# Optimization experiments

Measured on AMD Instinct MI355X. Metric: run time of the kernel, lower is better.

Reference implementation:

```python
import jax, jax.numpy as jnp
import numpy as np

NUM_HEADS = 6

def setup_inputs() -> dict:
    key = jax.random.key(0)
    k1, k2, k3, k4 = jax.random.split(key, 4)
    B, N, C = 8, 2048, 384
    x = jax.random.normal(k1, (B, N, C), dtype=jnp.float32)
    qkv_w = jax.random.normal(k2, (3 * C, C), dtype=jnp.float32) * (C ** -0.5)
    proj_w = jax.random.normal(k3, (C, C), dtype=jnp.float32) * (C ** -0.5)
    proj_b = jax.random.normal(k4, (C,), dtype=jnp.float32) * 0.01
    temperature = jnp.ones((NUM_HEADS, 1, 1), dtype=jnp.float32)
    return {"x": x, "qkv_w": qkv_w, "proj_w": proj_w, "proj_b": proj_b,
            "temperature": temperature}


def reference(x, qkv_w, proj_w, proj_b, temperature):
    B, N, C = x.shape
    H = NUM_HEADS
    Dh = C // H
    # qkv projection (no bias), split into q, k, v per head
    qkv = (x @ qkv_w.T).reshape(B, N, 3, H, Dh)
    qkv = jnp.transpose(qkv, (2, 0, 3, 1, 4))  # [3, B, H, N, Dh]
    q, k, v = qkv[0], qkv[1], qkv[2]
    # scores scaled by sqrt(C) (full dim, as in source), then learnable temperature
    attn = jnp.einsum('bhnd,bhmd->bhnm', q, k) / (C ** 0.5)
    attn = attn / temperature  # temperature: [H,1,1] broadcasts over B and N,N
    # diagonal (self-token) mask -> -inf before softmax
    diag = jnp.eye(N, dtype=bool)
    attn = jnp.where(diag, -jnp.inf, attn)
    attn = jax.nn.softmax(attn, axis=-1)
    # attend and merge heads
    out = jnp.einsum('bhnm,bhmd->bhnd', attn, v)
    out = jnp.transpose(out, (0, 2, 1, 3)).reshape(B, N, C)
    # output projection
    return out @ proj_w.T + proj_b
```

## Files before the change

### kernel.cpp

```cpp
#include <hip/hip_runtime.h>


using f32x4 = __attribute__((ext_vector_type(4))) float;
using s16x8 = __attribute__((ext_vector_type(8))) short;
using u16x4 = __attribute__((ext_vector_type(4))) unsigned short;
using u32x2 = __attribute__((ext_vector_type(2))) unsigned int;
using u32x4 = __attribute__((ext_vector_type(4))) unsigned int;
typedef unsigned short u16;
typedef unsigned int u32;

#define MFMA16(a, b, c) __builtin_amdgcn_mfma_f32_16x16x32_bf16(a, b, c, 0, 0, 0)
#define LOG2E 1.4426950408889634f
#define SQRTC 19.595917942265423f

__device__ __forceinline__ u16 f2bf(float f) {
  u32 u = __float_as_uint(f);
  u += 0x7fffu + ((u >> 16) & 1u);
  return (u16)(u >> 16);
}

__device__ __forceinline__ u32 cvtpk(float lo, float hi) {
  u32 r;
  asm("v_cvt_pk_bf16_f32 %0, %1, %2" : "=v"(r) : "v"(lo), "v"(hi));
  return r;
}

__device__ __forceinline__ float fexp2(float x) {
  float r;
  asm("v_exp_f32 %0, %1" : "=v"(r) : "v"(x));
  return r;
}

__device__ __forceinline__ void gld16(const void* g, void* l) {
  __builtin_amdgcn_global_load_lds((const __attribute__((address_space(1))) void*)g,
                                   (__attribute__((address_space(3))) void*)l, 16, 0, 0);
}

__global__ __launch_bounds__(256) void k_cvt(const float* __restrict__ in,
                                             u16* __restrict__ out) {
  const size_t i = (size_t)blockIdx.x * 256 + threadIdx.x;
  f32x4 v = *(const f32x4*)(in + i * 4);
  u16x4 o;
  o[0] = f2bf(v[0]); o[1] = f2bf(v[1]); o[2] = f2bf(v[2]); o[3] = f2bf(v[3]);
  *(u16x4*)(out + i * 4) = o;
}

__global__ __launch_bounds__(256) void k_qkv(const float* __restrict__ X,
                                             const u16* __restrict__ W,
                                             const float* __restrict__ temp,
                                             u16* __restrict__ Qb,
                                             u16* __restrict__ Kb,
                                             u16* __restrict__ Vt) {
  __shared__ u16 As[2][128 * 32];
  __shared__ u16 Bs[2][128 * 32];
  const int tid = threadIdx.x, w = tid >> 6, l = tid & 63, lr = l & 15, lg = l >> 4;
  const int tn = blockIdx.x * 128, tm = blockIdx.y * 128;
  const int wr = w >> 1, wc = w & 1;
  const int r0 = tid >> 2, c8 = (tid & 3) * 8;
  const int ar = tid >> 1, ac = (tid & 1) * 16;

  f32x4 acc[4][4] = {};
  f32x4 a4[4];

  auto issueA = [&](int kt) {
    const float* xp = X + (size_t)(tm + ar) * 384 + kt * 32 + ac;
    a4[0] = *(const f32x4*)(xp);
    a4[1] = *(const f32x4*)(xp + 4);
    a4[2] = *(const f32x4*)(xp + 8);
    a4[3] = *(const f32x4*)(xp + 12);
  };
  auto commitA = [&](int buf) {
    u32x4 h0, h1;
    h0[0] = cvtpk(a4[0][0], a4[0][1]); h0[1] = cvtpk(a4[0][2], a4[0][3]);
    h0[2] = cvtpk(a4[1][0], a4[1][1]); h0[3] = cvtpk(a4[1][2], a4[1][3]);
    h1[0] = cvtpk(a4[2][0], a4[2][1]); h1[1] = cvtpk(a4[2][2], a4[2][3]);
    h1[2] = cvtpk(a4[3][0], a4[3][1]); h1[3] = cvtpk(a4[3][2], a4[3][3]);
    *(u32x4*)&As[buf][ar * 32 + ac] = h0;
    *(u32x4*)&As[buf][ar * 32 + ac + 8] = h1;
  };
  auto stageB = [&](int buf, int kt) {
    const int k0 = kt * 32;
    char* db = (char*)(&Bs[buf][0]) + (w << 10);
    gld16(W + (size_t)(tn + r0) * 384 + k0 + c8, db);
    gld16(W + (size_t)(tn + 64 + r0) * 384 + k0 + c8, db + 4096);
  };

  issueA(0); stageB(0, 0); commitA(0);
  for (int kt = 0; kt < 12; ++kt) {
    __syncthreads();
    if (kt < 11) { issueA(kt + 1); stageB((kt + 1) & 1, kt + 1); }
    const int buf = kt & 1;
    s16x8 af[4], bfr[4];
    for (int mi = 0; mi < 4; mi++)
      af[mi] = *(const s16x8*)&As[buf][(wr * 64 + mi * 16 + lr) * 32 + lg * 8];
    for (int ni = 0; ni < 4; ni++)
      bfr[ni] = *(const s16x8*)&Bs[buf][(wc * 64 + ni * 16 + lr) * 32 + lg * 8];
    for (int mi = 0; mi < 4; mi++)
      for (int ni = 0; ni < 4; ni++)
        acc[mi][ni] = MFMA16(af[mi], bfr[ni], acc[mi][ni]);
    if (kt < 11) commitA((kt + 1) & 1);
  }

  const int which = (tn + wc * 64) / 384;
  const int bidx = (tm >> 11);
  for (int mi = 0; mi < 4; mi++)
    for (int ni = 0; ni < 4; ni++) {
      const int n = tn + wc * 64 + ni * 16 + lr;
      const int c = n - which * 384;
      const int h = c >> 6, d = c & 63;
      const size_t bh = (size_t)(bidx * 6 + h);
      if (which == 2) {
        const int pos0 = (tm + wr * 64 + mi * 16 + lg * 4) & 2047;
        u16x4 vv;
        vv[0] = f2bf(acc[mi][ni][0]); vv[1] = f2bf(acc[mi][ni][1]);
        vv[2] = f2bf(acc[mi][ni][2]); vv[3] = f2bf(acc[mi][ni][3]);
        *(u16x4*)&Vt[(bh * 64 + d) * 2048 + pos0] = vv;
      } else {
        const float mult = (which == 0) ? (LOG2E / (SQRTC * temp[h])) : 1.0f;
        for (int j = 0; j < 4; j++) {
          const int pos = (tm + wr * 64 + mi * 16 + lg * 4 + j) & 2047;
          const u16 val = f2bf(acc[mi][ni][j] * mult);
          if (which == 0) Qb[(bh * 2048 + pos) * 64 + d] = val;
          else            Kb[(bh * 2048 + pos) * 64 + d] = val;
        }
      }
    }
}

#define LDSOFF(row, c16) (((row) * 128 + (c16) * 16) ^ (((row) & 7) << 4))

__global__ __launch_bounds__(256, 3) void k_attn(const u16* __restrict__ Qb,
                                                 const u16* __restrict__ Kb,
                                                 const u16* __restrict__ Vt,
                                                 u16* __restrict__ AO) {
  __shared__ u16 Ks[2][64 * 64];
  __shared__ u16 Vs[2][64 * 64];
  __shared__ u16 Ps[4][32 * 72];
  const int tid = threadIdx.x, w = tid >> 6, l = tid & 63, lr = l & 15, lg = l >> 4;
  const int orig = blockIdx.x;
  const int rm = (orig & 7) * 96 + (orig >> 3);
  const int qt = rm & 15, bh = rm >> 4;
  const int h = bh % 6, b = bh / 6;
  const size_t base = (size_t)bh << 17;
  const int q0 = qt * 128 + w * 32;
  const int maskKt = q0 >> 6;
  const int qo = q0 & 63;

  s16x8 qf[2][2];
  for (int mi = 0; mi < 2; mi++)
    for (int ks = 0; ks < 2; ks++)
      qf[mi][ks] = *(const s16x8*)&Qb[base + (size_t)(q0 + mi * 16 + lr) * 64 + ks * 32 + lg * 8];

  s16x8 ones;
  for (int e = 0; e < 8; ++e) ones[e] = (short)0x3F80;

  f32x4 o0[4] = {}, o1[4] = {};
  f32x4 os0 = {}, os1 = {};

  const int r0 = tid >> 3, c0 = tid & 7;
  const int c8 = c0 * 8;
  const int wo0 = LDSOFF(r0, c0), wo1 = LDSOFF(r0 + 32, c0);

  s16x8 ka0, ka1, va0, va1;
  auto issue = [&](int kt) {
    const u16* kp = Kb + base + (size_t)(kt * 64 + r0) * 64 + c8;
    ka0 = *(const s16x8*)kp;
    ka1 = *(const s16x8*)(kp + 32 * 64);
    const u16* vp = Vt + base + (size_t)r0 * 2048 + kt * 64 + c8;
    va0 = *(const s16x8*)vp;
    va1 = *(const s16x8*)(vp + 32 * 2048);
  };
  auto commit = [&](int buf) {
    char* kd = (char*)&Ks[buf][0];
    char* vd = (char*)&Vs[buf][0];
    *(s16x8*)(kd + wo0) = ka0; *(s16x8*)(kd + wo1) = ka1;
    *(s16x8*)(vd + wo0) = va0; *(s16x8*)(vd + wo1) = va1;
  };

  issue(0); commit(0);
  __syncthreads();

  const int lrs = (lr & 7) << 4;
  const int x0 = (lg * 16) ^ lrs;
  const int x1 = (64 + lg * 16) ^ lrs;

  for (int kt = 0; kt < 32; ++kt) {
    const int cur = kt & 1;
    if (kt < 31) issue(kt + 1);

    f32x4 st0[4] = {}, st1[4] = {};
    const char* kbp = (const char*)&Ks[cur][0];
    __builtin_amdgcn_s_setprio(1);
    for (int ni = 0; ni < 4; ++ni) {
      const int rb = (ni * 16 + lr) * 128;
      const s16x8 kf0 = *(const s16x8*)(kbp + (rb + x0));
      const s16x8 kf1 = *(const s16x8*)(kbp + (rb + x1));
      st0[ni] = MFMA16(kf0, qf[0][0], st0[ni]);
      st0[ni] = MFMA16(kf1, qf[0][1], st0[ni]);
      st1[ni] = MFMA16(kf0, qf[1][0], st1[ni]);
      st1[ni] = MFMA16(kf1, qf[1][1], st1[ni]);
    }
    __builtin_amdgcn_s_setprio(0);

    if (kt == maskKt) {
      for (int ni = 0; ni < 4; ++ni)
        for (int j = 0; j < 4; ++j) {
          const int kvl = ni * 16 + lg * 4 + j;
          if (kvl == qo + lr)      st0[ni][j] = -1e30f;
          if (kvl == qo + 16 + lr) st1[ni][j] = -1e30f;
        }
    }

    const char* vbp = (const char*)&Vs[cur][0];
    s16x8 vfr[2][4];
    for (int ks = 0; ks < 2; ++ks) {
      const int xk = ks ? x1 : x0;
      for (int dj = 0; dj < 4; ++dj)
        vfr[ks][dj] = *(const s16x8*)(vbp + ((dj * 16 + lr) * 128 + xk));
    }

    u16* const psw = &Ps[w][0];
    {
      u16* pr = psw + lr * 72 + lg * 4;
      for (int ni = 0; ni < 4; ++ni) {
        u32x2 d2;
        d2[0] = cvtpk(fexp2(st0[ni][0]), fexp2(st0[ni][1]));
        d2[1] = cvtpk(fexp2(st0[ni][2]), fexp2(st0[ni][3]));
        *(u32x2*)(pr + ni * 16) = d2;
      }
    }
    {
      const s16x8 pa0k0 = *(const s16x8*)((const char*)(psw + lr * 72) + 0 * 64 + lg * 16);
      const s16x8 pa0k1 = *(const s16x8*)((const char*)(psw + lr * 72) + 1 * 64 + lg * 16);
      __builtin_amdgcn_s_setprio(1);
      for (int dj = 0; dj < 4; ++dj) o0[dj] = MFMA16(pa0k0, vfr[0][dj], o0[dj]);
      os0 = MFMA16(pa0k0, ones, os0);
      for (int dj = 0; dj < 4; ++dj) o0[dj] = MFMA16(pa0k1, vfr[1][dj], o0[dj]);
      os0 = MFMA16(pa0k1, ones, os0);
      __builtin_amdgcn_s_setprio(0);
    }
    {
      u16* pr = psw + (16 + lr) * 72 + lg * 4;
      for (int ni = 0; ni < 4; ++ni) {
        u32x2 d2;
        d2[0] = cvtpk(fexp2(st1[ni][0]), fexp2(st1[ni][1]));
        d2[1] = cvtpk(fexp2(st1[ni][2]), fexp2(st1[ni][3]));
        *(u32x2*)(pr + ni * 16) = d2;
      }
    }
    {
      const s16x8 pa1k0 = *(const s16x8*)((const char*)(psw + (16 + lr) * 72) + 0 * 64 + lg * 16);
      const s16x8 pa1k1 = *(const s16x8*)((const char*)(psw + (16 + lr) * 72) + 1 * 64 + lg * 16);
      __builtin_amdgcn_s_setprio(1);
      for (int dj = 0; dj < 4; ++dj) o1[dj] = MFMA16(pa1k0, vfr[0][dj], o1[dj]);
      os1 = MFMA16(pa1k0, ones, os1);
      for (int dj = 0; dj < 4; ++dj) o1[dj] = MFMA16(pa1k1, vfr[1][dj], o1[dj]);
      os1 = MFMA16(pa1k1, ones, os1);
      __builtin_amdgcn_s_setprio(0);
    }

    if (kt < 31) commit(cur ^ 1);
    __syncthreads();
  }

  f32x4 rv0, rv1;
  for (int j = 0; j < 4; ++j) { rv0[j] = 1.0f / os0[j]; rv1[j] = 1.0f / os1[j]; }
  const size_t aobase = (size_t)b * 2048 * 384 + (size_t)h * 64;
  for (int j = 0; j < 4; ++j) {
    const int pos0 = q0 + lg * 4 + j;
    const int pos1 = pos0 + 16;
    for (int dj = 0; dj < 4; ++dj) {
      AO[aobase + (size_t)pos0 * 384 + dj * 16 + lr] = f2bf(o0[dj][j] * rv0[j]);
      AO[aobase + (size_t)pos1 * 384 + dj * 16 + lr] = f2bf(o1[dj][j] * rv1[j]);
    }
  }
}

__global__ __launch_bounds__(256) void k_proj(const u16* __restrict__ A,
                                              const u16* __restrict__ W,
                                              const float* __restrict__ bias,
                                              float* __restrict__ out) {
  __shared__ u16 As[2][128 * 32];
  __shared__ u16 Bs[2][128 * 32];
  const int tid = threadIdx.x, w = tid >> 6, l = tid & 63, lr = l & 15, lg = l >> 4;
  const int tn = blockIdx.x * 128, tm = blockIdx.y * 128;
  const int wr = w >> 1, wc = w & 1;
  const int r0 = tid >> 2, c8 = (tid & 3) * 8;

  f32x4 acc[4][4] = {};

  auto stage = [&](int buf, int kt) {
    const int k0 = kt * 32;
    char* da = (char*)(&As[buf][0]) + (w << 10);
    char* db = (char*)(&Bs[buf][0]) + (w << 10);
    gld16(A + (size_t)(tm + r0) * 384 + k0 + c8, da);
    gld16(A + (size_t)(tm + 64 + r0) * 384 + k0 + c8, da + 4096);
    gld16(W + (size_t)(tn + r0) * 384 + k0 + c8, db);
    gld16(W + (size_t)(tn + 64 + r0) * 384 + k0 + c8, db + 4096);
  };

  stage(0, 0);
  for (int kt = 0; kt < 12; ++kt) {
    __syncthreads();
    if (kt < 11) stage((kt + 1) & 1, kt + 1);
    const int buf = kt & 1;
    s16x8 af[4], bfr[4];
    for (int mi = 0; mi < 4; mi++)
      af[mi] = *(const s16x8*)&As[buf][(wr * 64 + mi * 16 + lr) * 32 + lg * 8];
    for (int ni = 0; ni < 4; ni++)
      bfr[ni] = *(const s16x8*)&Bs[buf][(wc * 64 + ni * 16 + lr) * 32 + lg * 8];
    for (int mi = 0; mi < 4; mi++)
      for (int ni = 0; ni < 4; ni++)
        acc[mi][ni] = MFMA16(af[mi], bfr[ni], acc[mi][ni]);
  }

  for (int mi = 0; mi < 4; mi++)
    for (int ni = 0; ni < 4; ni++) {
      const int n = tn + wc * 64 + ni * 16 + lr;
      const float bn = bias[n];
      for (int j = 0; j < 4; j++) {
        const int m = tm + wr * 64 + mi * 16 + lg * 4 + j;
        out[(size_t)m * 384 + n] = acc[mi][ni][j] + bn;
      }
    }
}

extern "C" void kernel_launch(void* const* d_in, const int* in_sizes, int n_in,
                              void* d_out, int out_size, void* d_ws, size_t ws_size,
                              hipStream_t stream) {
  const float* x      = (const float*)d_in[0];
  const float* qkv_w  = (const float*)d_in[1];
  const float* proj_w = (const float*)d_in[2];
  const float* proj_b = (const float*)d_in[3];
  const float* temp   = (const float*)d_in[4];
  float* out = (float*)d_out;

  u16* wqkvb  = (u16*)d_ws;
  u16* wprojb = wqkvb + 442368;
  u16* Qb     = wprojb + 147456;
  u16* Kb     = Qb + 6291456;
  u16* Vtb    = Kb + 6291456;
  u16* AOb    = Vtb + 6291456;

  k_cvt<<<432, 256, 0, stream>>>(qkv_w, wqkvb);
  k_cvt<<<144, 256, 0, stream>>>(proj_w, wprojb);
  k_qkv<<<dim3(9, 128), 256, 0, stream>>>(x, wqkvb, temp, Qb, Kb, Vtb);
  k_attn<<<768, 256, 0, stream>>>(Qb, Kb, Vtb, AOb);
  k_proj<<<dim3(3, 128), 256, 0, stream>>>(AOb, wprojb, proj_b, out);
}
```

Measured before the change: 133.3 us.

## Fuse weight casts, transpose Q store, swizzle GEMM grids, shrink proj tile

The two weight-conversion launches are merged into one kernel. The QKV GEMM now writes Q transposed with vectorized 4-element stores, like V, and its block order is swizzled for cache locality. The attention kernel reads Q with strided scalar gathers, but only once per block. The projection GEMM moves to 128x64 tiles with a swizzled grid to double the block count, trading more A reloads for better occupancy and load balance.

Result: faster. 121.8 us (-8.6%).

```diff
diff --git a/kernel.cpp b/kernel.cpp
--- a/kernel.cpp
+++ b/kernel.cpp
@@ -36,9 +36,16 @@
                                    (__attribute__((address_space(3))) void*)l, 16, 0, 0);
 }
 
-__global__ __launch_bounds__(256) void k_cvt(const float* __restrict__ in,
-                                             u16* __restrict__ out) {
-  const size_t i = (size_t)blockIdx.x * 256 + threadIdx.x;
+__global__ __launch_bounds__(256) void k_cvt2(const float* __restrict__ A,
+                                              u16* __restrict__ Oa,
+                                              const float* __restrict__ B,
+                                              u16* __restrict__ Ob) {
+  const int bid = blockIdx.x;
+  const float* in;
+  u16* out;
+  size_t i;
+  if (bid < 432) { in = A; out = Oa; i = (size_t)bid * 256 + threadIdx.x; }
+  else           { in = B; out = Ob; i = (size_t)(bid - 432) * 256 + threadIdx.x; }
   f32x4 v = *(const f32x4*)(in + i * 4);
   u16x4 o;
   o[0] = f2bf(v[0]); o[1] = f2bf(v[1]); o[2] = f2bf(v[2]); o[3] = f2bf(v[3]);
@@ -48,13 +55,15 @@
 __global__ __launch_bounds__(256) void k_qkv(const float* __restrict__ X,
                                              const u16* __restrict__ W,
                                              const float* __restrict__ temp,
-                                             u16* __restrict__ Qb,
+                                             u16* __restrict__ Qt,
                                              u16* __restrict__ Kb,
                                              u16* __restrict__ Vt) {
   __shared__ u16 As[2][128 * 32];
   __shared__ u16 Bs[2][128 * 32];
   const int tid = threadIdx.x, w = tid >> 6, l = tid & 63, lr = l & 15, lg = l >> 4;
-  const int tn = blockIdx.x * 128, tm = blockIdx.y * 128;
+  const int id = blockIdx.y * 9 + blockIdx.x;
+  const int swz = (id & 7) * 144 + (id >> 3);
+  const int tn = (swz % 9) * 128, tm = (swz / 9) * 128;
   const int wr = w >> 1, wc = w & 1;
   const int r0 = tid >> 2, c8 = (tid & 3) * 8;
   const int ar = tid >> 1, ac = (tid & 1) * 16;
@@ -109,27 +118,26 @@
       const int c = n - which * 384;
       const int h = c >> 6, d = c & 63;
       const size_t bh = (size_t)(bidx * 6 + h);
-      if (which == 2) {
+      if (which == 1) {
+        for (int j = 0; j < 4; j++) {
+          const int pos = (tm + wr * 64 + mi * 16 + lg * 4 + j) & 2047;
+          Kb[(bh * 2048 + pos) * 64 + d] = f2bf(acc[mi][ni][j]);
+        }
+      } else {
+        const float mult = (which == 0) ? (LOG2E / (SQRTC * temp[h])) : 1.0f;
         const int pos0 = (tm + wr * 64 + mi * 16 + lg * 4) & 2047;
         u16x4 vv;
-        vv[0] = f2bf(acc[mi][ni][0]); vv[1] = f2bf(acc[mi][ni][1]);
-        vv[2] = f2bf(acc[mi][ni][2]); vv[3] = f2bf(acc[mi][ni][3]);
-        *(u16x4*)&Vt[(bh * 64 + d) * 2048 + pos0] = vv;
-      } else {
-        const float mult = (which == 0) ? (LOG2E / (SQRTC * temp[h])) : 1.0f;
-        for (int j = 0; j < 4; j++) {
-          const int pos = (tm + wr * 64 + mi * 16 + lg * 4 + j) & 2047;
-          const u16 val = f2bf(acc[mi][ni][j] * mult);
-          if (which == 0) Qb[(bh * 2048 + pos) * 64 + d] = val;
-          else            Kb[(bh * 2048 + pos) * 64 + d] = val;
-        }
+        vv[0] = f2bf(acc[mi][ni][0] * mult); vv[1] = f2bf(acc[mi][ni][1] * mult);
+        vv[2] = f2bf(acc[mi][ni][2] * mult); vv[3] = f2bf(acc[mi][ni][3] * mult);
+        u16* dst = (which == 0) ? Qt : Vt;
+        *(u16x4*)&dst[(bh * 64 + d) * 2048 + pos0] = vv;
       }
     }
 }
 
 #define LDSOFF(row, c16) (((row) * 128 + (c16) * 16) ^ (((row) & 7) << 4))
 
-__global__ __launch_bounds__(256, 3) void k_attn(const u16* __restrict__ Qb,
+__global__ __launch_bounds__(256, 3) void k_attn(const u16* __restrict__ Qt,
                                                  const u16* __restrict__ Kb,
                                                  const u16* __restrict__ Vt,
                                                  u16* __restrict__ AO) {
@@ -148,8 +156,12 @@
 
   s16x8 qf[2][2];
   for (int mi = 0; mi < 2; mi++)
-    for (int ks = 0; ks < 2; ks++)
-      qf[mi][ks] = *(const s16x8*)&Qb[base + (size_t)(q0 + mi * 16 + lr) * 64 + ks * 32 + lg * 8];
+    for (int ks = 0; ks < 2; ks++) {
+      const u16* qp = Qt + base + (size_t)(ks * 32 + lg * 8) * 2048 + q0 + mi * 16 + lr;
+      s16x8 q;
+      for (int e = 0; e < 8; ++e) q[e] = (short)qp[(size_t)e * 2048];
+      qf[mi][ks] = q;
+    }
 
   s16x8 ones;
   for (int e = 0; e < 8; ++e) ones[e] = (short)0x3F80;
@@ -281,13 +293,14 @@
                                               const float* __restrict__ bias,
                                               float* __restrict__ out) {
   __shared__ u16 As[2][128 * 32];
-  __shared__ u16 Bs[2][128 * 32];
+  __shared__ u16 Bs[2][64 * 32];
   const int tid = threadIdx.x, w = tid >> 6, l = tid & 63, lr = l & 15, lg = l >> 4;
-  const int tn = blockIdx.x * 128, tm = blockIdx.y * 128;
-  const int wr = w >> 1, wc = w & 1;
+  const int id = blockIdx.y * 6 + blockIdx.x;
+  const int swz = (id & 7) * 96 + (id >> 3);
+  const int tn = (swz % 6) * 64, tm = (swz / 6) * 128;
   const int r0 = tid >> 2, c8 = (tid & 3) * 8;
 
-  f32x4 acc[4][4] = {};
+  f32x4 acc[2][4] = {};
 
   auto stage = [&](int buf, int kt) {
     const int k0 = kt * 32;
@@ -296,7 +309,6 @@
     gld16(A + (size_t)(tm + r0) * 384 + k0 + c8, da);
     gld16(A + (size_t)(tm + 64 + r0) * 384 + k0 + c8, da + 4096);
     gld16(W + (size_t)(tn + r0) * 384 + k0 + c8, db);
-    gld16(W + (size_t)(tn + 64 + r0) * 384 + k0 + c8, db + 4096);
   };
 
   stage(0, 0);
@@ -304,22 +316,22 @@
     __syncthreads();
     if (kt < 11) stage((kt + 1) & 1, kt + 1);
     const int buf = kt & 1;
-    s16x8 af[4], bfr[4];
-    for (int mi = 0; mi < 4; mi++)
-      af[mi] = *(const s16x8*)&As[buf][(wr * 64 + mi * 16 + lr) * 32 + lg * 8];
+    s16x8 af[2], bfr[4];
+    for (int mi = 0; mi < 2; mi++)
+      af[mi] = *(const s16x8*)&As[buf][(w * 32 + mi * 16 + lr) * 32 + lg * 8];
     for (int ni = 0; ni < 4; ni++)
-      bfr[ni] = *(const s16x8*)&Bs[buf][(wc * 64 + ni * 16 + lr) * 32 + lg * 8];
-    for (int mi = 0; mi < 4; mi++)
+      bfr[ni] = *(const s16x8*)&Bs[buf][(ni * 16 + lr) * 32 + lg * 8];
+    for (int mi = 0; mi < 2; mi++)
       for (int ni = 0; ni < 4; ni++)
         acc[mi][ni] = MFMA16(af[mi], bfr[ni], acc[mi][ni]);
   }
 
-  for (int mi = 0; mi < 4; mi++)
+  for (int mi = 0; mi < 2; mi++)
     for (int ni = 0; ni < 4; ni++) {
-      const int n = tn + wc * 64 + ni * 16 + lr;
+      const int n = tn + ni * 16 + lr;
       const float bn = bias[n];
       for (int j = 0; j < 4; j++) {
-        const int m = tm + wr * 64 + mi * 16 + lg * 4 + j;
+        const int m = tm + w * 32 + mi * 16 + lg * 4 + j;
         out[(size_t)m * 384 + n] = acc[mi][ni][j] + bn;
       }
     }
@@ -337,14 +349,13 @@
 
   u16* wqkvb  = (u16*)d_ws;
   u16* wprojb = wqkvb + 442368;
-  u16* Qb     = wprojb + 147456;
-  u16* Kb     = Qb + 6291456;
+  u16* Qt     = wprojb + 147456;
+  u16* Kb     = Qt + 6291456;
   u16* Vtb    = Kb + 6291456;
   u16* AOb    = Vtb + 6291456;
 
-  k_cvt<<<432, 256, 0, stream>>>(qkv_w, wqkvb);
-  k_cvt<<<144, 256, 0, stream>>>(proj_w, wprojb);
-  k_qkv<<<dim3(9, 128), 256, 0, stream>>>(x, wqkvb, temp, Qb, Kb, Vtb);
-  k_attn<<<768, 256, 0, stream>>>(Qb, Kb, Vtb, AOb);
-  k_proj<<<dim3(3, 128), 256, 0, stream>>>(AOb, wprojb, proj_b, out);
-}
+  k_cvt2<<<576, 256, 0, stream>>>(qkv_w, wqkvb, proj_w, wprojb);
+  k_qkv<<<dim3(9, 128), 256, 0, stream>>>(x, wqkvb, temp, Qt, Kb, Vtb);
+  k_attn<<<768, 256, 0, stream>>>(Qt, Kb, Vtb, AOb);
+  k_proj<<<dim3(6, 128), 256, 0, stream>>>(AOb, wprojb, proj_b, out);
+}
```
